# Kernel tuning notes

Measured on AMD Instinct MI355X. Metric: run time of the kernel, lower is better.

The kernel has to match this reference:

```python
import jax, jax.numpy as jnp
import numpy as np

N_NODES = 100000
N_EDGES = 3200000
D_FEAT = 16


def scatter_mean(src, index, num_segments):
    # src: [E, d], index: [E] -> [num_segments, d]; mean over incident edges,
    # with count clamped to 1 (matches torch_scatter.scatter_mean behavior).
    sums = jax.ops.segment_sum(src, index, num_segments=num_segments)
    counts = jax.ops.segment_sum(jnp.ones((src.shape[0],), dtype=src.dtype), index,
                                 num_segments=num_segments)
    return sums / jnp.maximum(counts, 1.0)[:, None]


def setup_inputs() -> dict:
    key = jax.random.key(0)
    k1, k2, k3 = jax.random.split(key, 3)
    predictedTensor = jax.random.normal(k1, (N_NODES, D_FEAT), dtype=jnp.float32)
    inputTensor = jax.random.normal(k2, (N_NODES, D_FEAT), dtype=jnp.float32)
    edge_index = jax.random.randint(k3, (2, N_EDGES), 0, N_NODES, dtype=jnp.int64)
    return {"predictedTensor": predictedTensor, "inputTensor": inputTensor,
            "edge_index": edge_index}


def reference(predictedTensor, inputTensor, edge_index):
    row, col = edge_index[0], edge_index[1]
    n = predictedTensor.shape[0]
    delta_dash = scatter_mean(predictedTensor[row] - predictedTensor[col], row, n)
    delta = scatter_mean(inputTensor[row] - inputTensor[col], row, n)
    diff = delta_dash - delta                      # [N, d]
    return jnp.mean(jnp.sum(diff * diff, axis=1))  # scalar
```

## Files before the change

kernel.cpp:

```cpp
#include <hip/hip_runtime.h>

#define NN 100000
#define CSH 7
#define CNODES 128
#define NC ((NN + CNODES - 1) / CNODES)
#define TPB 256
#define TPBS 512
#define TPBB 512
#define EPQ 4
#define TILE4 (TPBS * EPQ)
#define TILEE (TILE4 * 4)
#define PADG 16u
#define SEGMAXP 7168
#define SENT 0xFFFFFFFFu

__device__ __forceinline__ unsigned f2bf(float f) {
    unsigned u = __float_as_uint(f);
    return (u + 0x7FFFu + ((u >> 16) & 1u)) >> 16;
}
__device__ __forceinline__ unsigned pk(float lo, float hi) {
    return f2bf(lo) | (f2bf(hi) << 16);
}
__device__ __forceinline__ float bflo(unsigned v) { return __uint_as_float(v << 16); }
__device__ __forceinline__ float bfhi(unsigned v) { return __uint_as_float(v & 0xFFFF0000u); }

__global__ void k_q(const float4* __restrict__ pred, const float4* __restrict__ inp,
                    uint4* __restrict__ qb, unsigned* __restrict__ cursor,
                    float* __restrict__ out, int n8) {
    int i = blockIdx.x * blockDim.x + threadIdx.x;
    if (i < NC) cursor[i] = 0u;
    if (i == 0) *out = 0.f;
    if (i < n8) {
        float4 a0 = pred[2 * i], a1 = pred[2 * i + 1];
        float4 b0 = inp[2 * i],  b1 = inp[2 * i + 1];
        uint4 o;
        o.x = pk(a0.x - b0.x, a0.y - b0.y);
        o.y = pk(a0.z - b0.z, a0.w - b0.w);
        o.z = pk(a1.x - b1.x, a1.y - b1.y);
        o.w = pk(a1.z - b1.z, a1.w - b1.w);
        qb[i] = o;
    }
}

__global__ __launch_bounds__(TPBS) void k_scat1(const int4* __restrict__ row4,
                        const int4* __restrict__ col4,
                        const int* __restrict__ row, const int* __restrict__ col,
                        unsigned* __restrict__ cursor, unsigned* __restrict__ binned, int E) {
    __shared__ unsigned lcnt[NC], lofs[NC], lpos[NC], gdst[NC];
    __shared__ unsigned stage[TILEE];
    __shared__ unsigned sscan[TPBS];
    int tid = threadIdx.x;
    int E4 = E >> 2;
    long long base4 = (long long)blockIdx.x * TILE4;
    bool lastblk = (blockIdx.x == gridDim.x - 1);
    for (int i = tid; i < NC; i += TPBS) { lcnt[i] = 0u; lpos[i] = 0u; }
    __syncthreads();
    int4 r[EPQ], c[EPQ];
    bool val[EPQ];
    #pragma unroll
    for (int j = 0; j < EPQ; ++j) {
        long long i4 = base4 + (long long)j * TPBS + tid;
        val[j] = (i4 < E4);
        if (val[j]) {
            r[j] = row4[i4]; c[j] = col4[i4];
            atomicAdd(&lcnt[((unsigned)r[j].x) >> CSH], 1u);
            atomicAdd(&lcnt[((unsigned)r[j].y) >> CSH], 1u);
            atomicAdd(&lcnt[((unsigned)r[j].z) >> CSH], 1u);
            atomicAdd(&lcnt[((unsigned)r[j].w) >> CSH], 1u);
        }
    }
    int rt = 0, ct_ = 0;
    bool tval = lastblk && tid < (E & 3);
    if (tval) {
        int e = (E & ~3) + tid;
        rt = row[e]; ct_ = col[e];
        atomicAdd(&lcnt[((unsigned)rt) >> CSH], 1u);
    }
    __syncthreads();
    unsigned v0 = (2 * tid     < NC) ? lcnt[2 * tid]     : 0u;
    unsigned v1 = (2 * tid + 1 < NC) ? lcnt[2 * tid + 1] : 0u;
    unsigned s = v0 + v1;
    sscan[tid] = s;
    __syncthreads();
    for (int off = 1; off < TPBS; off <<= 1) {
        unsigned t = (tid >= off) ? sscan[tid - off] : 0u;
        __syncthreads();
        sscan[tid] += t;
        __syncthreads();
    }
    unsigned ex = sscan[tid] - s;
    if (2 * tid < NC) {
        lofs[2 * tid] = ex;
        unsigned rp = (v0 + PADG - 1u) & ~(PADG - 1u);
        gdst[2 * tid] = rp ? atomicAdd(&cursor[2 * tid], rp) : 0u;
    }
    if (2 * tid + 1 < NC) {
        lofs[2 * tid + 1] = ex + v0;
        unsigned rp = (v1 + PADG - 1u) & ~(PADG - 1u);
        gdst[2 * tid + 1] = rp ? atomicAdd(&cursor[2 * tid + 1], rp) : 0u;
    }
    __syncthreads();
    #pragma unroll
    for (int j = 0; j < EPQ; ++j) {
        if (val[j]) {
            int rr[4] = {r[j].x, r[j].y, r[j].z, r[j].w};
            int cc4[4] = {c[j].x, c[j].y, c[j].z, c[j].w};
            #pragma unroll
            for (int k = 0; k < 4; ++k) {
                unsigned ru = (unsigned)rr[k];
                unsigned b = ru >> CSH;
                unsigned pos = lofs[b] + atomicAdd(&lpos[b], 1u);
                stage[pos] = ((ru & (CNODES - 1u)) << 17) | (unsigned)cc4[k];
            }
        }
    }
    if (tval) {
        unsigned ru = (unsigned)rt;
        unsigned b = ru >> CSH;
        unsigned pos = lofs[b] + atomicAdd(&lpos[b], 1u);
        stage[pos] = ((ru & (CNODES - 1u)) << 17) | (unsigned)ct_;
    }
    __syncthreads();
    for (int i = tid; i < NC; i += TPBS) {
        unsigned cc = lcnt[i];
        unsigned rp = (cc + PADG - 1u) & ~(PADG - 1u);
        unsigned ls = lofs[i];
        unsigned gd = gdst[i];
        if (gd + rp > SEGMAXP) rp = (gd < SEGMAXP) ? (SEGMAXP - gd) : 0u;
        uint4* dst = (uint4*)(binned + (size_t)i * SEGMAXP + gd);
        for (unsigned j = 0; j < rp; j += 4u) {
            uint4 v;
            v.x = (j + 0 < cc) ? stage[ls + j + 0] : SENT;
            v.y = (j + 1 < cc) ? stage[ls + j + 1] : SENT;
            v.z = (j + 2 < cc) ? stage[ls + j + 2] : SENT;
            v.w = (j + 3 < cc) ? stage[ls + j + 3] : SENT;
            dst[j >> 2] = v;
        }
    }
}

__global__ __launch_bounds__(TPBB) void k_bucket(const uint2* __restrict__ qb2,
                         const uint4* __restrict__ binned4,
                         const unsigned* __restrict__ cursor,
                         float* __restrict__ out, int N) {
    __shared__ unsigned ncnt[CNODES], nstart[CNODES], ncur[CNODES];
    __shared__ unsigned scol[SEGMAXP];
    __shared__ float wred[8];
    int tid = threadIdx.x, b = blockIdx.x;
    if (tid < CNODES) ncnt[tid] = 0u;
    __syncthreads();
    const uint4* seg4 = binned4 + (size_t)b * (SEGMAXP / 4);
    unsigned m = cursor[b];
    if (m > SEGMAXP) m = SEGMAXP;
    unsigned m4 = m >> 2;
    for (unsigned i = tid; i < m4; i += TPBB) {
        uint4 v = seg4[i];
        if (v.x != SENT) atomicAdd(&ncnt[v.x >> 17], 1u);
        if (v.y != SENT) atomicAdd(&ncnt[v.y >> 17], 1u);
        if (v.z != SENT) atomicAdd(&ncnt[v.z >> 17], 1u);
        if (v.w != SENT) atomicAdd(&ncnt[v.w >> 17], 1u);
    }
    __syncthreads();
    if (tid < 64) {
        unsigned c0 = ncnt[tid * 2], c1 = ncnt[tid * 2 + 1];
        unsigned s = c0 + c1;
        unsigned x = s;
        #pragma unroll
        for (int off = 1; off < 64; off <<= 1) {
            unsigned t = __shfl_up(x, off);
            if (tid >= off) x += t;
        }
        unsigned ex = x - s;
        nstart[tid * 2] = ex;          ncur[tid * 2] = ex;
        nstart[tid * 2 + 1] = ex + c0; ncur[tid * 2 + 1] = ex + c0;
    }
    __syncthreads();
    for (unsigned i = tid; i < m4; i += TPBB) {
        uint4 v = seg4[i];
        if (v.x != SENT) { unsigned rk = atomicAdd(&ncur[v.x >> 17], 1u); scol[rk] = v.x & 0x1FFFFu; }
        if (v.y != SENT) { unsigned rk = atomicAdd(&ncur[v.y >> 17], 1u); scol[rk] = v.y & 0x1FFFFu; }
        if (v.z != SENT) { unsigned rk = atomicAdd(&ncur[v.z >> 17], 1u); scol[rk] = v.z & 0x1FFFFu; }
        if (v.w != SENT) { unsigned rk = atomicAdd(&ncur[v.w >> 17], 1u); scol[rk] = v.w & 0x1FFFFu; }
    }
    __syncthreads();

    int nl = tid >> 2;
    int p  = tid & 3;
    int wid = tid >> 6, lane = tid & 63;
    int n = (b << CSH) + nl;
    unsigned cnt = ncnt[nl], st = nstart[nl];
    float a0 = 0.f, a1 = 0.f, a2 = 0.f, a3 = 0.f;
    unsigned i = 0;
    for (; i + 2 <= cnt; i += 2) {
        unsigned cA = scol[st + i];
        unsigned cB = scol[st + i + 1];
        uint2 vA = qb2[(size_t)cA * 4 + p];
        uint2 vB = qb2[(size_t)cB * 4 + p];
        a0 += bflo(vA.x); a1 += bfhi(vA.x); a2 += bflo(vA.y); a3 += bfhi(vA.y);
        a0 += bflo(vB.x); a1 += bfhi(vB.x); a2 += bflo(vB.y); a3 += bfhi(vB.y);
    }
    if (i < cnt) {
        unsigned cA = scol[st + i];
        uint2 vA = qb2[(size_t)cA * 4 + p];
        a0 += bflo(vA.x); a1 += bfhi(vA.x); a2 += bflo(vA.y); a3 += bfhi(vA.y);
    }
    float ss = 0.f;
    if (n < N) {
        uint2 v = qb2[(size_t)n * 4 + p];
        float cf = (float)cnt;
        float d0 = cf * bflo(v.x) - a0, d1 = cf * bfhi(v.x) - a1;
        float d2 = cf * bflo(v.y) - a2, d3 = cf * bfhi(v.y) - a3;
        ss = d0 * d0 + d1 * d1 + d2 * d2 + d3 * d3;
    }
    ss += __shfl_xor(ss, 1);
    ss += __shfl_xor(ss, 2);
    float bss = 0.f;
    if (p == 0 && n < N) {
        float c1f = (cnt > 1u) ? (float)cnt : 1.f;
        bss = ss / (c1f * c1f);
    }
    #pragma unroll
    for (int mm = 4; mm < 64; mm <<= 1) bss += __shfl_xor(bss, mm);
    if (lane == 0) wred[wid] = bss;
    __syncthreads();
    if (tid == 0) {
        float acc = 0.f;
        #pragma unroll
        for (int w = 0; w < 8; ++w) acc += wred[w];
        atomicAdd(out, acc * (1.0f / (float)NN));
    }
}

extern "C" void kernel_launch(void* const* d_in, const int* in_sizes, int n_in,
                              void* d_out, int out_size, void* d_ws, size_t ws_size,
                              hipStream_t stream) {
    const float* pred = (const float*)d_in[0];
    const float* inp  = (const float*)d_in[1];
    const int*   eidx = (const int*)d_in[2];

    const int N = NN;
    const int E = in_sizes[2] / 2;
    const int* row = eidx;
    const int* col = eidx + E;

    size_t off = 0;
    auto alloc = [&](size_t bytes) { void* p = (char*)d_ws + off; off = (off + bytes + 511) & ~(size_t)511; return p; };
    uint4*    qb     = (uint4*)alloc((size_t)N * 32);
    unsigned* cursor = (unsigned*)alloc(NC * sizeof(unsigned));
    unsigned* binned = (unsigned*)alloc((size_t)NC * SEGMAXP * sizeof(unsigned));

    int n8 = N * 16 / 8;
    k_q<<<(n8 + TPB - 1) / TPB, TPB, 0, stream>>>((const float4*)pred, (const float4*)inp,
                                                  qb, cursor, (float*)d_out, n8);

    int E4 = E >> 2;
    int nsc = (E4 + TILE4 - 1) / TILE4;
    k_scat1<<<nsc, TPBS, 0, stream>>>((const int4*)row, (const int4*)col, row, col,
                                      cursor, binned, E);

    k_bucket<<<NC, TPBB, 0, stream>>>((const uint2*)qb, (const uint4*)binned, cursor,
                                      (float*)d_out, N);
}
```

Before: 74.36 us.

## Use wave-level shuffle scan and per-wave counters with register-held items in bucket kernel

In the scatter kernel, the barrier-heavy shared-memory prefix scan is replaced by a wavefront shuffle scan plus a small cross-wave offset step, cutting many __syncthreads. In the bucket kernel, each thread loads its binned entries into registers once (ITK slots cover the whole segment) instead of reading global memory twice. Histogram counters are split per wave, with per-wave offsets derived afterwards, which reduces LDS atomic contention. The cost is more registers and shared memory, which may lower occupancy.

```diff
diff --git a/kernel.cpp b/kernel.cpp
--- a/kernel.cpp
+++ b/kernel.cpp
@@ -12,6 +12,8 @@
 #define TILEE (TILE4 * 4)
 #define PADG 16u
 #define SEGMAXP 7168
+#define SEGMAXP4 (SEGMAXP / 4)
+#define ITK 4
 #define SENT 0xFFFFFFFFu
 
 __device__ __forceinline__ unsigned f2bf(float f) {
@@ -48,8 +50,9 @@
                         unsigned* __restrict__ cursor, unsigned* __restrict__ binned, int E) {
     __shared__ unsigned lcnt[NC], lofs[NC], lpos[NC], gdst[NC];
     __shared__ unsigned stage[TILEE];
-    __shared__ unsigned sscan[TPBS];
+    __shared__ unsigned wtot[8], wofs[8];
     int tid = threadIdx.x;
+    int lane = tid & 63, wid = tid >> 6;
     int E4 = E >> 2;
     long long base4 = (long long)blockIdx.x * TILE4;
     bool lastblk = (blockIdx.x == gridDim.x - 1);
@@ -80,15 +83,25 @@
     unsigned v0 = (2 * tid     < NC) ? lcnt[2 * tid]     : 0u;
     unsigned v1 = (2 * tid + 1 < NC) ? lcnt[2 * tid + 1] : 0u;
     unsigned s = v0 + v1;
-    sscan[tid] = s;
-    __syncthreads();
-    for (int off = 1; off < TPBS; off <<= 1) {
-        unsigned t = (tid >= off) ? sscan[tid - off] : 0u;
-        __syncthreads();
-        sscan[tid] += t;
-        __syncthreads();
-    }
-    unsigned ex = sscan[tid] - s;
+    unsigned x = s;
+    #pragma unroll
+    for (int off = 1; off < 64; off <<= 1) {
+        unsigned t = __shfl_up(x, off);
+        if (lane >= off) x += t;
+    }
+    if (lane == 63) wtot[wid] = x;
+    __syncthreads();
+    if (tid < 8) {
+        unsigned wv = wtot[tid], wx = wv;
+        #pragma unroll
+        for (int off = 1; off < 8; off <<= 1) {
+            unsigned t = __shfl_up(wx, off);
+            if (tid >= off) wx += t;
+        }
+        wofs[tid] = wx - wv;
+    }
+    __syncthreads();
+    unsigned ex = x - s + wofs[wid];
     if (2 * tid < NC) {
         lofs[2 * tid] = ex;
         unsigned rp = (v0 + PADG - 1u) & ~(PADG - 1u);
@@ -143,22 +156,42 @@
                          const uint4* __restrict__ binned4,
                          const unsigned* __restrict__ cursor,
                          float* __restrict__ out, int N) {
-    __shared__ unsigned ncnt[CNODES], nstart[CNODES], ncur[CNODES];
+    __shared__ unsigned ncnt8[8][CNODES];
+    __shared__ unsigned ncnt[CNODES], nstart[CNODES];
     __shared__ unsigned scol[SEGMAXP];
     __shared__ float wred[8];
     int tid = threadIdx.x, b = blockIdx.x;
-    if (tid < CNODES) ncnt[tid] = 0u;
-    __syncthreads();
-    const uint4* seg4 = binned4 + (size_t)b * (SEGMAXP / 4);
+    int lane = tid & 63, wid = tid >> 6;
+    for (int i = tid; i < 8 * CNODES; i += TPBB) ((unsigned*)ncnt8)[i] = 0u;
+    __syncthreads();
+    const uint4* seg4 = binned4 + (size_t)b * SEGMAXP4;
     unsigned m = cursor[b];
     if (m > SEGMAXP) m = SEGMAXP;
     unsigned m4 = m >> 2;
-    for (unsigned i = tid; i < m4; i += TPBB) {
-        uint4 v = seg4[i];
-        if (v.x != SENT) atomicAdd(&ncnt[v.x >> 17], 1u);
-        if (v.y != SENT) atomicAdd(&ncnt[v.y >> 17], 1u);
-        if (v.z != SENT) atomicAdd(&ncnt[v.z >> 17], 1u);
-        if (v.w != SENT) atomicAdd(&ncnt[v.w >> 17], 1u);
+    uint4 it[ITK];
+    bool hv[ITK];
+    #pragma unroll
+    for (int k = 0; k < ITK; ++k) {
+        unsigned idx = (unsigned)tid + (unsigned)k * TPBB;
+        hv[k] = (idx < m4);
+        if (hv[k]) {
+            it[k] = seg4[idx];
+            if (it[k].x != SENT) atomicAdd(&ncnt8[wid][it[k].x >> 17], 1u);
+            if (it[k].y != SENT) atomicAdd(&ncnt8[wid][it[k].y >> 17], 1u);
+            if (it[k].z != SENT) atomicAdd(&ncnt8[wid][it[k].z >> 17], 1u);
+            if (it[k].w != SENT) atomicAdd(&ncnt8[wid][it[k].w >> 17], 1u);
+        }
+    }
+    __syncthreads();
+    if (tid < CNODES) {
+        unsigned t0 = 0u;
+        #pragma unroll
+        for (int w = 0; w < 8; ++w) {
+            unsigned c = ncnt8[w][tid];
+            ncnt8[w][tid] = t0;
+            t0 += c;
+        }
+        ncnt[tid] = t0;
     }
     __syncthreads();
     if (tid < 64) {
@@ -171,22 +204,29 @@
             if (tid >= off) x += t;
         }
         unsigned ex = x - s;
-        nstart[tid * 2] = ex;          ncur[tid * 2] = ex;
-        nstart[tid * 2 + 1] = ex + c0; ncur[tid * 2 + 1] = ex + c0;
-    }
-    __syncthreads();
-    for (unsigned i = tid; i < m4; i += TPBB) {
-        uint4 v = seg4[i];
-        if (v.x != SENT) { unsigned rk = atomicAdd(&ncur[v.x >> 17], 1u); scol[rk] = v.x & 0x1FFFFu; }
-        if (v.y != SENT) { unsigned rk = atomicAdd(&ncur[v.y >> 17], 1u); scol[rk] = v.y & 0x1FFFFu; }
-        if (v.z != SENT) { unsigned rk = atomicAdd(&ncur[v.z >> 17], 1u); scol[rk] = v.z & 0x1FFFFu; }
-        if (v.w != SENT) { unsigned rk = atomicAdd(&ncur[v.w >> 17], 1u); scol[rk] = v.w & 0x1FFFFu; }
+        nstart[tid * 2] = ex;
+        nstart[tid * 2 + 1] = ex + c0;
+    }
+    __syncthreads();
+    if (tid < CNODES) {
+        unsigned ns = nstart[tid];
+        #pragma unroll
+        for (int w = 0; w < 8; ++w) ncnt8[w][tid] += ns;
+    }
+    __syncthreads();
+    #pragma unroll
+    for (int k = 0; k < ITK; ++k) {
+        if (hv[k]) {
+            if (it[k].x != SENT) { unsigned rk = atomicAdd(&ncnt8[wid][it[k].x >> 17], 1u); scol[rk] = it[k].x & 0x1FFFFu; }
+            if (it[k].y != SENT) { unsigned rk = atomicAdd(&ncnt8[wid][it[k].y >> 17], 1u); scol[rk] = it[k].y & 0x1FFFFu; }
+            if (it[k].z != SENT) { unsigned rk = atomicAdd(&ncnt8[wid][it[k].z >> 17], 1u); scol[rk] = it[k].z & 0x1FFFFu; }
+            if (it[k].w != SENT) { unsigned rk = atomicAdd(&ncnt8[wid][it[k].w >> 17], 1u); scol[rk] = it[k].w & 0x1FFFFu; }
+        }
     }
     __syncthreads();
 
     int nl = tid >> 2;
     int p  = tid & 3;
-    int wid = tid >> 6, lane = tid & 63;
     int n = (b << CSH) + nl;
     unsigned cnt = ncnt[nl], st = nstart[nl];
     float a0 = 0.f, a1 = 0.f, a2 = 0.f, a3 = 0.f;
```

New measurement: 73.88 us. No clear change (-0.6%).
